# Kernel tuning notes

Hardware: AMD Instinct MI355X
Metric: run time of the kernel (lower is better)

Reference implementation:

```python
import jax, jax.numpy as jnp
import numpy as np

N = 100000      # nodes
E = 1600000     # directed edges (before self-loops)
DIN = 128       # input feature dim
HID = 32        # per-head hidden dim
HEADS = 4
D1 = HID * HEADS  # 128, concat width
NG = 64         # graphs in batch
NEG_SLOPE = 0.2 # PyG GATConv leaky_relu slope


def setup_inputs() -> dict:
    key = jax.random.key(0)
    ks = jax.random.split(key, 16)
    s = 0.05
    x = jax.random.normal(ks[0], (N, DIN), dtype=jnp.float32)
    edge_index = jax.random.randint(ks[1], (2, E), 0, N, dtype=jnp.int32)
    batch = jnp.sort(jax.random.randint(ks[2], (N,), 0, NG, dtype=jnp.int32))
    # GATConv 1: in=DIN, out=HID, heads=HEADS, concat=True
    W1 = jax.random.normal(ks[3], (D1, DIN), dtype=jnp.float32) * s
    a1s = jax.random.normal(ks[4], (HEADS, HID), dtype=jnp.float32) * s
    a1d = jax.random.normal(ks[5], (HEADS, HID), dtype=jnp.float32) * s
    b1 = jnp.zeros((D1,), jnp.float32)
    # GATConv 2: in=D1, out=HID, heads=HEADS, concat=True
    W2 = jax.random.normal(ks[6], (D1, D1), dtype=jnp.float32) * s
    a2s = jax.random.normal(ks[7], (HEADS, HID), dtype=jnp.float32) * s
    a2d = jax.random.normal(ks[8], (HEADS, HID), dtype=jnp.float32) * s
    b2 = jnp.zeros((D1,), jnp.float32)
    # GATConv 3: in=D1, out=HID, heads=HEADS, concat=False (mean over heads)
    W3 = jax.random.normal(ks[9], (D1, D1), dtype=jnp.float32) * s
    a3s = jax.random.normal(ks[10], (HEADS, HID), dtype=jnp.float32) * s
    a3d = jax.random.normal(ks[11], (HEADS, HID), dtype=jnp.float32) * s
    b3 = jnp.zeros((HID,), jnp.float32)
    lin_w = jax.random.normal(ks[12], (1, HID), dtype=jnp.float32) * s
    lin_b = jnp.zeros((1,), jnp.float32)
    return {"x": x, "edge_index": edge_index, "batch": batch,
            "W1": W1, "a1s": a1s, "a1d": a1d, "b1": b1,
            "W2": W2, "a2s": a2s, "a2d": a2d, "b2": b2,
            "W3": W3, "a3s": a3s, "a3d": a3d, "b3": b3,
            "lin_w": lin_w, "lin_b": lin_b}


def _gat_conv(x, ei, W, att_src, att_dst, bias, concat):
    """PyG GATConv (no edge features, self-loops already in ei)."""
    n = x.shape[0]
    h = (x @ W.T).reshape(n, HEADS, HID)          # [N, H, C]
    src, dst = ei[0], ei[1]
    a_src = jnp.einsum('nhc,hc->nh', h, att_src)  # [N, H]
    a_dst = jnp.einsum('nhc,hc->nh', h, att_dst)
    e = jax.nn.leaky_relu(a_src[src] + a_dst[dst], NEG_SLOPE)  # [Etot, H]
    # segment softmax over incoming edges of each dst node
    e_max = jax.ops.segment_max(e, dst, num_segments=n)
    ex = jnp.exp(e - e_max[dst])
    denom = jax.ops.segment_sum(ex, dst, num_segments=n)
    alpha = ex / denom[dst]                        # [Etot, H]
    out = jax.ops.segment_sum(h[src] * alpha[:, :, None], dst, num_segments=n)
    if concat:
        out = out.reshape(n, HEADS * HID)
    else:
        out = out.mean(axis=1)
    return out + bias


def reference(x, edge_index, batch, W1, a1s, a1d, b1, W2, a2s, a2d, b2,
              W3, a3s, a3d, b3, lin_w, lin_b):
    loops = jnp.arange(N, dtype=edge_index.dtype)
    ei = jnp.concatenate([edge_index, jnp.stack([loops, loops])], axis=1)
    h = jax.nn.elu(_gat_conv(x, ei, W1, a1s, a1d, b1, True))
    h = jax.nn.elu(_gat_conv(h, ei, W2, a2s, a2d, b2, True))
    h = jax.nn.elu(_gat_conv(h, ei, W3, a3s, a3d, b3, False))
    h = h @ lin_w.T + lin_b                        # [N, 1]
    counts = jax.ops.segment_sum(jnp.ones((N,), h.dtype), batch, num_segments=NG)
    pooled = jax.ops.segment_sum(h, batch, num_segments=NG) / counts[:, None]
    return pooled.squeeze()                        # [NG]
```

## Files before the change

kernel.cpp:

```cpp
#include <hip/hip_runtime.h>
#include <hip/hip_fp16.h>
#include <math.h>

#define D1 128
#define NEG 0.2f
#define NODE_SHIFT 9
#define BIN_NODES 512
#define MAXBIN 256

typedef short v8s __attribute__((ext_vector_type(8)));
typedef float v4f __attribute__((ext_vector_type(4)));

__device__ __forceinline__ float lrelu(float v){ return v > 0.f ? v : NEG * v; }
__device__ __forceinline__ float elu_f(float v){ return v > 0.f ? v : __expf(v) - 1.f; }

__device__ __forceinline__ unsigned short bf16s(float f){
    unsigned u = __float_as_uint(f);
    return (unsigned short)((u + 0x7fffu + ((u >> 16) & 1u)) >> 16);
}
__device__ __forceinline__ float bf2f(unsigned short s){
    return __uint_as_float(((unsigned)s) << 16);
}
__device__ __forceinline__ unsigned f2h2(float a, float b){
    return ((unsigned)__half_as_ushort(__float2half_rn(b)) << 16) |
           (unsigned)__half_as_ushort(__float2half_rn(a));
}
__device__ __forceinline__ float2 h2f2(unsigned u){
    float lo = __half2float(__ushort_as_half((unsigned short)(u & 0xffffu)));
    float hi = __half2float(__ushort_as_half((unsigned short)(u >> 16)));
    return make_float2(lo, hi);
}
__device__ __forceinline__ void split8(const float* f, v8s& hi, v8s& lo){
    #pragma unroll
    for (int i = 0; i < 8; i++){
        unsigned short h = bf16s(f[i]);
        ((short*)&hi)[i] = (short)h;
        ((short*)&lo)[i] = (short)bf16s(f[i] - bf2f(h));
    }
}


__global__ __launch_bounds__(256) void kb_hist(const int* __restrict__ ei,
                                               int* __restrict__ binCnt,
                                               int n_edges, int etot, int nbin){
    __shared__ int h[MAXBIN];
    for (int i = threadIdx.x; i < nbin; i += 256) h[i] = 0;
    __syncthreads();
    int stride = gridDim.x * 256;
    for (int e = blockIdx.x * 256 + threadIdx.x; e < etot; e += stride){
        int dst = (e < n_edges) ? ei[n_edges + e] : (e - n_edges);
        atomicAdd(&h[dst >> NODE_SHIFT], 1);
    }
    __syncthreads();
    for (int i = threadIdx.x; i < nbin; i += 256)
        if (h[i]) atomicAdd(&binCnt[i], h[i]);
}

__global__ void kb_scan(const int* __restrict__ binCnt, int* __restrict__ binStart,
                        int* __restrict__ binCursor, int nbin,
                        int* __restrict__ rowptr, int n_nodes, int etot){
    if (threadIdx.x == 0){
        int run = 0;
        for (int b = 0; b < nbin; b++){
            binStart[b] = run; binCursor[b] = run; run += binCnt[b];
        }
        binStart[nbin] = run;
        rowptr[n_nodes] = etot;
    }
}

__global__ __launch_bounds__(256) void kb_scatter(const int* __restrict__ ei,
                                                  int* __restrict__ binCursor,
                                                  uint2* __restrict__ staged,
                                                  int n_edges, int etot, int nbin){
    __shared__ int cnt[MAXBIN];
    __shared__ int base[MAXBIN];
    int e0 = blockIdx.x * 4096;
    for (int i = threadIdx.x; i < nbin; i += 256) cnt[i] = 0;
    __syncthreads();
    #pragma unroll 4
    for (int r = 0; r < 16; r++){
        int e = e0 + r * 256 + threadIdx.x;
        if (e < etot){
            int dst = (e < n_edges) ? ei[n_edges + e] : (e - n_edges);
            atomicAdd(&cnt[dst >> NODE_SHIFT], 1);
        }
    }
    __syncthreads();
    for (int i = threadIdx.x; i < nbin; i += 256){
        base[i] = cnt[i] ? atomicAdd(&binCursor[i], cnt[i]) : 0;
        cnt[i] = 0;
    }
    __syncthreads();
    #pragma unroll 4
    for (int r = 0; r < 16; r++){
        int e = e0 + r * 256 + threadIdx.x;
        if (e < etot){
            int src, dst;
            if (e < n_edges){ src = ei[e]; dst = ei[n_edges + e]; }
            else            { src = dst = e - n_edges; }
            int b = dst >> NODE_SHIFT;
            int p = base[b] + atomicAdd(&cnt[b], 1);
            staged[p] = make_uint2((unsigned)src, (unsigned)dst);
        }
    }
}

__global__ __launch_bounds__(512) void kb_final(const uint2* __restrict__ staged,
                                                const int* __restrict__ binStart,
                                                int* __restrict__ rowptr,
                                                int* __restrict__ eidx, int n_nodes){
    __shared__ int deg[BIN_NODES];
    __shared__ int cur[BIN_NODES];
    int b = blockIdx.x;
    int nbase = b << NODE_SHIFT;
    int s0 = binStart[b], s1 = binStart[b + 1];
    deg[threadIdx.x] = 0;
    __syncthreads();
    for (int i = s0 + threadIdx.x; i < s1; i += 512)
        atomicAdd(&deg[staged[i].y & (BIN_NODES - 1)], 1);
    __syncthreads();
    int v = deg[threadIdx.x];
    cur[threadIdx.x] = v;
    __syncthreads();
    for (int off = 1; off < BIN_NODES; off <<= 1){
        int t = (threadIdx.x >= off) ? cur[threadIdx.x - off] : 0;
        __syncthreads();
        cur[threadIdx.x] += t;
        __syncthreads();
    }
    int excl = cur[threadIdx.x] - v;
    int node = nbase + threadIdx.x;
    if (node < n_nodes) rowptr[node] = s0 + excl;
    cur[threadIdx.x] = s0 + excl;
    __syncthreads();
    for (int i = s0 + threadIdx.x; i < s1; i += 512){
        uint2 pr = staged[i];
        int p = atomicAdd(&cur[pr.y & (BIN_NODES - 1)], 1);
        eidx[p] = (int)pr.x;
    }
}


__global__ void k_prepw(const float* __restrict__ W1, const float* __restrict__ W2,
                        const float* __restrict__ W3, unsigned short* __restrict__ Bp){
    int t = blockIdx.x * 256 + threadIdx.x;
    if (t >= 49152) return;
    int w = t >> 14;
    int r = t & 16383;
    int k = r >> 7, j = r & 127;
    const float* W = (w == 0) ? W1 : (w == 1) ? W2 : W3;
    float val = W[j * 128 + k];
    unsigned short hi = bf16s(val);
    unsigned short lo = bf16s(val - bf2f(hi));
    int idx = (k >> 3) * 1024 + j * 8 + (k & 7);
    Bp[w * 32768 + idx] = hi;
    Bp[w * 32768 + 16384 + idx] = lo;
}


template<int FP32SRC>
__global__ __launch_bounds__(256) void k_mgemm(
        const float* __restrict__ Xf,
        const unsigned short* __restrict__ Xhi, const unsigned short* __restrict__ Xlo,
        const unsigned short* __restrict__ Bp,
        const float* __restrict__ aw_s, const float* __restrict__ aw_d,
        unsigned short* __restrict__ Hh,
        float* __restrict__ asrc, float* __restrict__ adst, int n_rows){
    extern __shared__ unsigned short Bs[];
    int lane = threadIdx.x & 63;
    int li = lane & 15, quad = lane >> 4;
    int wv = threadIdx.x >> 6;
    int r0 = blockIdx.x * 128 + wv * 32;

    int row0 = r0 + li;
    int row1 = r0 + 16 + li;
    int rc0 = row0 < n_rows ? row0 : 0;
    int rc1 = row1 < n_rows ? row1 : 0;

    v8s ah0[4], al0[4], ah1[4], al1[4];
    #pragma unroll
    for (int ks = 0; ks < 4; ks++){
        int koff = ks * 32 + quad * 8;
        if (FP32SRC){
            float f0[8], f1[8];
            *(float4*)&f0[0] = *(const float4*)(Xf + (size_t)rc0 * 128 + koff);
            *(float4*)&f0[4] = *(const float4*)(Xf + (size_t)rc0 * 128 + koff + 4);
            *(float4*)&f1[0] = *(const float4*)(Xf + (size_t)rc1 * 128 + koff);
            *(float4*)&f1[4] = *(const float4*)(Xf + (size_t)rc1 * 128 + koff + 4);
            split8(f0, ah0[ks], al0[ks]);
            split8(f1, ah1[ks], al1[ks]);
        } else {
            ah0[ks] = *(const v8s*)(Xhi + (size_t)rc0 * 128 + koff);
            al0[ks] = *(const v8s*)(Xlo + (size_t)rc0 * 128 + koff);
            ah1[ks] = *(const v8s*)(Xhi + (size_t)rc1 * 128 + koff);
            al1[ks] = *(const v8s*)(Xlo + (size_t)rc1 * 128 + koff);
        }
    }

    #pragma unroll
    for (int i = 0; i < 16; i++){
        int idx = threadIdx.x + i * 256;
        ((float4*)Bs)[idx] = ((const float4*)Bp)[idx];
    }
    __syncthreads();

    v4f acc[2][8];
    #pragma unroll
    for (int m = 0; m < 2; m++)
        #pragma unroll
        for (int t = 0; t < 8; t++)
            acc[m][t] = (v4f){0.f, 0.f, 0.f, 0.f};

    #pragma unroll
    for (int ks = 0; ks < 4; ks++){
        #pragma unroll
        for (int t = 0; t < 8; t++){
            int bo = (ks * 4 + quad) * 1024 + (t * 16 + li) * 8;
            v8s bh = *(const v8s*)(Bs + bo);
            v8s bl = *(const v8s*)(Bs + 16384 + bo);
            acc[0][t] = __builtin_amdgcn_mfma_f32_16x16x32_bf16(ah0[ks], bh, acc[0][t], 0, 0, 0);
            acc[0][t] = __builtin_amdgcn_mfma_f32_16x16x32_bf16(ah0[ks], bl, acc[0][t], 0, 0, 0);
            acc[0][t] = __builtin_amdgcn_mfma_f32_16x16x32_bf16(al0[ks], bh, acc[0][t], 0, 0, 0);
            acc[1][t] = __builtin_amdgcn_mfma_f32_16x16x32_bf16(ah1[ks], bh, acc[1][t], 0, 0, 0);
            acc[1][t] = __builtin_amdgcn_mfma_f32_16x16x32_bf16(ah1[ks], bl, acc[1][t], 0, 0, 0);
            acc[1][t] = __builtin_amdgcn_mfma_f32_16x16x32_bf16(al1[ks], bh, acc[1][t], 0, 0, 0);
        }
    }

    #pragma unroll
    for (int m = 0; m < 2; m++){
        #pragma unroll
        for (int t = 0; t < 8; t++){
            #pragma unroll
            for (int r = 0; r < 4; r++){
                float v  = acc[m][t][r];
                float vo = __shfl_xor(v, 1);
                if (!(li & 1)){
                    int row = r0 + m * 16 + quad * 4 + r;
                    if (row < n_rows)
                        *(unsigned*)(Hh + (size_t)row * 128 + t * 16 + li) = f2h2(v, vo);
                }
            }
        }
    }

    float as8[8], ad8[8];
    #pragma unroll
    for (int t = 0; t < 8; t++){
        as8[t] = aw_s[t * 16 + li];
        ad8[t] = aw_d[t * 16 + li];
    }
    #pragma unroll
    for (int m = 0; m < 2; m++){
        #pragma unroll
        for (int r = 0; r < 4; r++){
            float sp[4], dp[4];
            #pragma unroll
            for (int h = 0; h < 4; h++){
                sp[h] = acc[m][2*h][r] * as8[2*h] + acc[m][2*h+1][r] * as8[2*h+1];
                dp[h] = acc[m][2*h][r] * ad8[2*h] + acc[m][2*h+1][r] * ad8[2*h+1];
            }
            #pragma unroll
            for (int off = 1; off < 16; off <<= 1){
                #pragma unroll
                for (int h = 0; h < 4; h++){
                    sp[h] += __shfl_xor(sp[h], off);
                    dp[h] += __shfl_xor(dp[h], off);
                }
            }
            if (li == 0){
                int row = r0 + m * 16 + quad * 4 + r;
                if (row < n_rows){
                    ((float4*)asrc)[row] = make_float4(sp[0], sp[1], sp[2], sp[3]);
                    ((float4*)adst)[row] = make_float4(dp[0], dp[1], dp[2], dp[3]);
                }
            }
        }
    }
}


template<int MEAN>
__global__ __launch_bounds__(256) void k_aggr(
        const unsigned* __restrict__ Hh,
        const float* __restrict__ asrc, const float* __restrict__ adst,
        const int* __restrict__ rowptr, const int* __restrict__ eidx,
        const float* __restrict__ bias,
        unsigned short* __restrict__ Oh, unsigned short* __restrict__ Ol,
        float* __restrict__ Of, int n_nodes){
    int lane = threadIdx.x & 63;
    int wid  = threadIdx.x >> 6;
    int n = blockIdx.x * 4 + wid;
    if (n >= n_nodes) return;
    int row0 = rowptr[n];
    int deg  = rowptr[n + 1] - row0;
    const int* ep = eidx + row0;
    unsigned hd = (unsigned)(lane >> 4);
    unsigned ul = (unsigned)lane;
    float4 ad = ((const float4*)adst)[n];
    float adh = hd == 0 ? ad.x : hd == 1 ? ad.y : hd == 2 ? ad.z : ad.w;
    unsigned wh = (ul >> 3) & 3;
    float adw = wh == 0 ? ad.x : wh == 1 ? ad.y : wh == 2 ? ad.z : ad.w;
    int wsrc = (int)(hd * 8);

    float accx = 0.f, accy = 0.f, den = 0.f;
    int i = 0;
    for (; i + 8 <= deg; i += 8){
        unsigned s[8];
        #pragma unroll
        for (int j = 0; j < 8; j++) s[j] = (unsigned)ep[i + j];
        float aW = asrc[s[ul & 7] * 4u + wh];
        float w = __expf(lrelu(aW + adw));
        unsigned hw[8];
        #pragma unroll
        for (int j = 0; j < 8; j++) hw[j] = Hh[s[j] * 64u + ul];
        #pragma unroll
        for (int j = 0; j < 8; j++){
            float wj = __shfl(w, wsrc + j);
            float2 hv = h2f2(hw[j]);
            den  += wj;
            accx += wj * hv.x;
            accy += wj * hv.y;
        }
    }
    for (; i < deg; i++){
        unsigned s = (unsigned)ep[i];
        float w = __expf(lrelu(asrc[s * 4u + hd] + adh));
        float2 hv = h2f2(Hh[s * 64u + ul]);
        den  += w;
        accx += w * hv.x;
        accy += w * hv.y;
    }
    float rdh = 1.f / den;
    accx *= rdh; accy *= rdh;

    int c = lane * 2;
    if (!MEAN){
        float ox = elu_f(accx + bias[c]);
        float oy = elu_f(accy + bias[c + 1]);
        unsigned short hx = bf16s(ox), hy = bf16s(oy);
        unsigned short lx = bf16s(ox - bf2f(hx)), ly = bf16s(oy - bf2f(hy));
        *(ushort2*)(Oh + (size_t)n * 128 + c) = make_ushort2(hx, hy);
        *(ushort2*)(Ol + (size_t)n * 128 + c) = make_ushort2(lx, ly);
    } else {
        float sx = accx, sy = accy;
        sx += __shfl_xor(sx, 16); sy += __shfl_xor(sy, 16);
        sx += __shfl_xor(sx, 32); sy += __shfl_xor(sy, 32);
        if (lane < 16){
            int cc = lane * 2;
            float ox = elu_f(sx * 0.25f + bias[cc]);
            float oy = elu_f(sy * 0.25f + bias[cc + 1]);
            *(float2*)(Of + (size_t)n * 32 + cc) = make_float2(ox, oy);
        }
    }
}


__global__ void k_readout(const float* __restrict__ H3, const int* __restrict__ batch,
                          const float* __restrict__ lw, const float* __restrict__ lb,
                          float* __restrict__ pool, float* __restrict__ cnt, int n_nodes){
    __shared__ float pl[64];
    __shared__ float cl[64];
    if (threadIdx.x < 64){ pl[threadIdx.x] = 0.f; cl[threadIdx.x] = 0.f; }
    __syncthreads();
    int n = blockIdx.x * 256 + threadIdx.x;
    if (n < n_nodes){
        const float4* hp = (const float4*)(H3 + (size_t)n * 32);
        const float4* wp = (const float4*)lw;
        float y = 0.f;
        #pragma unroll
        for (int i = 0; i < 8; i++){
            float4 h4 = hp[i], w4 = wp[i];
            y += h4.x * w4.x + h4.y * w4.y + h4.z * w4.z + h4.w * w4.w;
        }
        y += lb[0];
        int b = batch[n];
        atomicAdd(&pl[b], y);
        atomicAdd(&cl[b], 1.f);
    }
    __syncthreads();
    if (threadIdx.x < 64 && cl[threadIdx.x] != 0.f){
        atomicAdd(&pool[threadIdx.x], pl[threadIdx.x]);
        atomicAdd(&cnt[threadIdx.x], cl[threadIdx.x]);
    }
}

__global__ void k_final(const float* __restrict__ pool, const float* __restrict__ cnt,
                        float* __restrict__ out){
    int g = threadIdx.x;
    if (g < 64) out[g] = (cnt[g] > 0.f) ? pool[g] / cnt[g] : 0.f;
}


extern "C" void kernel_launch(void* const* d_in, const int* in_sizes, int n_in,
                              void* d_out, int out_size, void* d_ws, size_t ws_size,
                              hipStream_t stream){
    const float* x   = (const float*)d_in[0];
    const int*   ei  = (const int*)  d_in[1];
    const int*   bat = (const int*)  d_in[2];
    const float* W1  = (const float*)d_in[3];
    const float* a1s = (const float*)d_in[4];
    const float* a1d = (const float*)d_in[5];
    const float* b1  = (const float*)d_in[6];
    const float* W2  = (const float*)d_in[7];
    const float* a2s = (const float*)d_in[8];
    const float* a2d = (const float*)d_in[9];
    const float* b2  = (const float*)d_in[10];
    const float* W3  = (const float*)d_in[11];
    const float* a3s = (const float*)d_in[12];
    const float* a3d = (const float*)d_in[13];
    const float* b3  = (const float*)d_in[14];
    const float* lw  = (const float*)d_in[15];
    const float* lb  = (const float*)d_in[16];
    (void)n_in; (void)out_size; (void)ws_size;

    const int n_nodes = in_sizes[0] / D1;
    const int n_edges = in_sizes[1] / 2;
    const int etot    = n_edges + n_nodes;
    const int nbin    = (n_nodes + BIN_NODES - 1) >> NODE_SHIFT;

    char* p = (char*)d_ws;
    size_t off = 0;
    auto alloc = [&](size_t bytes) -> char* {
        char* r = p + off;
        off = (off + bytes + 511) & ~(size_t)511;
        return r;
    };
    unsigned short* Hh   = (unsigned short*)alloc((size_t)n_nodes * 128 * 2);
    unsigned short* Xhi  = (unsigned short*)alloc((size_t)n_nodes * 128 * 2);
    unsigned short* Xlo  = (unsigned short*)alloc((size_t)n_nodes * 128 * 2);
    float*          asrc = (float*)alloc((size_t)n_nodes * 4 * 4);
    float*          adst = (float*)alloc((size_t)n_nodes * 4 * 4);
    unsigned short* Bp   = (unsigned short*)alloc(3 * 32768 * 2);
    int*   rowptr  = (int*)alloc((size_t)(n_nodes + 1) * 4);
    int*   eidx    = (int*)alloc((size_t)etot * 4);
    uint2* staged  = (uint2*)alloc((size_t)etot * 8);
    int*   binCnt  = (int*)alloc(MAXBIN * 4);
    int*   binStart= (int*)alloc((MAXBIN + 1) * 4);
    int*   binCur  = (int*)alloc(MAXBIN * 4);
    float* pool    = (float*)alloc(64 * 4);
    float* cnt     = (float*)alloc(64 * 4);
    float* h3      = (float*)Xhi;

    hipMemsetAsync(binCnt, 0, MAXBIN * 4, stream);
    hipMemsetAsync(pool, 0, 64 * 4, stream);
    hipMemsetAsync(cnt, 0, 64 * 4, stream);

    k_prepw<<<192, 256, 0, stream>>>(W1, W2, W3, Bp);

    int cb = (etot + 4095) / 4096;
    kb_hist<<<cb, 256, 0, stream>>>(ei, binCnt, n_edges, etot, nbin);
    kb_scan<<<1, 64, 0, stream>>>(binCnt, binStart, binCur, nbin, rowptr, n_nodes, etot);
    kb_scatter<<<cb, 256, 0, stream>>>(ei, binCur, staged, n_edges, etot, nbin);
    kb_final<<<nbin, 512, 0, stream>>>(staged, binStart, rowptr, eidx, n_nodes);

    int mb = (n_nodes + 127) / 128;
    int rb = (n_nodes + 3) / 4;

    k_mgemm<1><<<mb, 256, 65536, stream>>>(x, nullptr, nullptr, Bp,
                                           a1s, a1d, Hh, asrc, adst, n_nodes);
    k_aggr<0><<<rb, 256, 0, stream>>>((const unsigned*)Hh, asrc, adst, rowptr, eidx,
                                      b1, Xhi, Xlo, nullptr, n_nodes);
    k_mgemm<0><<<mb, 256, 65536, stream>>>(nullptr, Xhi, Xlo, Bp + 32768,
                                           a2s, a2d, Hh, asrc, adst, n_nodes);
    k_aggr<0><<<rb, 256, 0, stream>>>((const unsigned*)Hh, asrc, adst, rowptr, eidx,
                                      b2, Xhi, Xlo, nullptr, n_nodes);
    k_mgemm<0><<<mb, 256, 65536, stream>>>(nullptr, Xhi, Xlo, Bp + 65536,
                                           a3s, a3d, Hh, asrc, adst, n_nodes);
    k_aggr<1><<<rb, 256, 0, stream>>>((const unsigned*)Hh, asrc, adst, rowptr, eidx,
                                      b3, nullptr, nullptr, h3, n_nodes);

    int ob = (n_nodes + 255) / 256;
    k_readout<<<ob, 256, 0, stream>>>(h3, bat, lw, lb, pool, cnt, n_nodes);
    k_final<<<1, 64, 0, stream>>>(pool, cnt, (float*)d_out);
}
```

Baseline: 572.8 us.

## Pack staged edges into 32-bit words and halve GEMM shared memory via K-staging

The CSR build now packs each staged edge as the local destination (9 bits) and the source (17 bits) into one 32-bit word, halving the staged buffer's traffic. The GEMM stops holding all four K-slices of the A operand in registers and stops keeping the full 64KB B matrix in LDS. It instead loads B in two 32KB halves, with a sync between them, and loads the A fragments per K-step. The aim is higher occupancy (launch_bounds 256,4) at the cost of an extra barrier and serialized B loads. The packing assumes node ids fit in 17 bits (below 131072).

Measured after the change: 545.7 us. -4.7%, faster.

```diff
diff --git a/kernel.cpp b/kernel.cpp
--- a/kernel.cpp
+++ b/kernel.cpp
@@ -71,7 +71,7 @@
 
 __global__ __launch_bounds__(256) void kb_scatter(const int* __restrict__ ei,
                                                   int* __restrict__ binCursor,
-                                                  uint2* __restrict__ staged,
+                                                  unsigned* __restrict__ staged,
                                                   int n_edges, int etot, int nbin){
     __shared__ int cnt[MAXBIN];
     __shared__ int base[MAXBIN];
@@ -101,12 +101,12 @@
             else            { src = dst = e - n_edges; }
             int b = dst >> NODE_SHIFT;
             int p = base[b] + atomicAdd(&cnt[b], 1);
-            staged[p] = make_uint2((unsigned)src, (unsigned)dst);
-        }
-    }
-}
-
-__global__ __launch_bounds__(512) void kb_final(const uint2* __restrict__ staged,
+            staged[p] = ((unsigned)(dst & (BIN_NODES - 1)) << 17) | (unsigned)src;
+        }
+    }
+}
+
+__global__ __launch_bounds__(512) void kb_final(const unsigned* __restrict__ staged,
                                                 const int* __restrict__ binStart,
                                                 int* __restrict__ rowptr,
                                                 int* __restrict__ eidx, int n_nodes){
@@ -118,7 +118,7 @@
     deg[threadIdx.x] = 0;
     __syncthreads();
     for (int i = s0 + threadIdx.x; i < s1; i += 512)
-        atomicAdd(&deg[staged[i].y & (BIN_NODES - 1)], 1);
+        atomicAdd(&deg[staged[i] >> 17], 1);
     __syncthreads();
     int v = deg[threadIdx.x];
     cur[threadIdx.x] = v;
@@ -135,9 +135,9 @@
     cur[threadIdx.x] = s0 + excl;
     __syncthreads();
     for (int i = s0 + threadIdx.x; i < s1; i += 512){
-        uint2 pr = staged[i];
-        int p = atomicAdd(&cur[pr.y & (BIN_NODES - 1)], 1);
-        eidx[p] = (int)pr.x;
+        unsigned pr = staged[i];
+        int p = atomicAdd(&cur[pr >> 17], 1);
+        eidx[p] = (int)(pr & 0x1FFFFu);
     }
 }
 
@@ -160,17 +160,17 @@
 
 
 template<int FP32SRC>
-__global__ __launch_bounds__(256) void k_mgemm(
+__global__ __launch_bounds__(256, 4) void k_mgemm(
         const float* __restrict__ Xf,
         const unsigned short* __restrict__ Xhi, const unsigned short* __restrict__ Xlo,
         const unsigned short* __restrict__ Bp,
         const float* __restrict__ aw_s, const float* __restrict__ aw_d,
         unsigned short* __restrict__ Hh,
         float* __restrict__ asrc, float* __restrict__ adst, int n_rows){
-    extern __shared__ unsigned short Bs[];
+    __shared__ unsigned short Bs[16384];
     int lane = threadIdx.x & 63;
+    int wv   = threadIdx.x >> 6;
     int li = lane & 15, quad = lane >> 4;
-    int wv = threadIdx.x >> 6;
     int r0 = blockIdx.x * 128 + wv * 32;
 
     int row0 = r0 + li;
@@ -178,33 +178,6 @@
     int rc0 = row0 < n_rows ? row0 : 0;
     int rc1 = row1 < n_rows ? row1 : 0;
 
-    v8s ah0[4], al0[4], ah1[4], al1[4];
-    #pragma unroll
-    for (int ks = 0; ks < 4; ks++){
-        int koff = ks * 32 + quad * 8;
-        if (FP32SRC){
-            float f0[8], f1[8];
-            *(float4*)&f0[0] = *(const float4*)(Xf + (size_t)rc0 * 128 + koff);
-            *(float4*)&f0[4] = *(const float4*)(Xf + (size_t)rc0 * 128 + koff + 4);
-            *(float4*)&f1[0] = *(const float4*)(Xf + (size_t)rc1 * 128 + koff);
-            *(float4*)&f1[4] = *(const float4*)(Xf + (size_t)rc1 * 128 + koff + 4);
-            split8(f0, ah0[ks], al0[ks]);
-            split8(f1, ah1[ks], al1[ks]);
-        } else {
-            ah0[ks] = *(const v8s*)(Xhi + (size_t)rc0 * 128 + koff);
-            al0[ks] = *(const v8s*)(Xlo + (size_t)rc0 * 128 + koff);
-            ah1[ks] = *(const v8s*)(Xhi + (size_t)rc1 * 128 + koff);
-            al1[ks] = *(const v8s*)(Xlo + (size_t)rc1 * 128 + koff);
-        }
-    }
-
-    #pragma unroll
-    for (int i = 0; i < 16; i++){
-        int idx = threadIdx.x + i * 256;
-        ((float4*)Bs)[idx] = ((const float4*)Bp)[idx];
-    }
-    __syncthreads();
-
     v4f acc[2][8];
     #pragma unroll
     for (int m = 0; m < 2; m++)
@@ -213,18 +186,46 @@
             acc[m][t] = (v4f){0.f, 0.f, 0.f, 0.f};
 
     #pragma unroll
-    for (int ks = 0; ks < 4; ks++){
-        #pragma unroll
-        for (int t = 0; t < 8; t++){
-            int bo = (ks * 4 + quad) * 1024 + (t * 16 + li) * 8;
-            v8s bh = *(const v8s*)(Bs + bo);
-            v8s bl = *(const v8s*)(Bs + 16384 + bo);
-            acc[0][t] = __builtin_amdgcn_mfma_f32_16x16x32_bf16(ah0[ks], bh, acc[0][t], 0, 0, 0);
-            acc[0][t] = __builtin_amdgcn_mfma_f32_16x16x32_bf16(ah0[ks], bl, acc[0][t], 0, 0, 0);
-            acc[0][t] = __builtin_amdgcn_mfma_f32_16x16x32_bf16(al0[ks], bh, acc[0][t], 0, 0, 0);
-            acc[1][t] = __builtin_amdgcn_mfma_f32_16x16x32_bf16(ah1[ks], bh, acc[1][t], 0, 0, 0);
-            acc[1][t] = __builtin_amdgcn_mfma_f32_16x16x32_bf16(ah1[ks], bl, acc[1][t], 0, 0, 0);
-            acc[1][t] = __builtin_amdgcn_mfma_f32_16x16x32_bf16(al1[ks], bh, acc[1][t], 0, 0, 0);
+    for (int g = 0; g < 2; g++){
+        if (g) __syncthreads();
+        #pragma unroll
+        for (int i = 0; i < 4; i++){
+            int idx = threadIdx.x + i * 256;
+            ((float4*)Bs)[idx]          = ((const float4*)(Bp + g * 8192))[idx];
+            ((float4*)(Bs + 8192))[idx] = ((const float4*)(Bp + 16384 + g * 8192))[idx];
+        }
+        __syncthreads();
+        #pragma unroll
+        for (int ks2 = 0; ks2 < 2; ks2++){
+            int ks = g * 2 + ks2;
+            int koff = ks * 32 + quad * 8;
+            v8s ah0, al0, ah1, al1;
+            if (FP32SRC){
+                float f0[8], f1[8];
+                *(float4*)&f0[0] = *(const float4*)(Xf + (size_t)rc0 * 128 + koff);
+                *(float4*)&f0[4] = *(const float4*)(Xf + (size_t)rc0 * 128 + koff + 4);
+                *(float4*)&f1[0] = *(const float4*)(Xf + (size_t)rc1 * 128 + koff);
+                *(float4*)&f1[4] = *(const float4*)(Xf + (size_t)rc1 * 128 + koff + 4);
+                split8(f0, ah0, al0);
+                split8(f1, ah1, al1);
+            } else {
+                ah0 = *(const v8s*)(Xhi + (size_t)rc0 * 128 + koff);
+                al0 = *(const v8s*)(Xlo + (size_t)rc0 * 128 + koff);
+                ah1 = *(const v8s*)(Xhi + (size_t)rc1 * 128 + koff);
+                al1 = *(const v8s*)(Xlo + (size_t)rc1 * 128 + koff);
+            }
+            #pragma unroll
+            for (int t = 0; t < 8; t++){
+                int bo = ks2 * 4096 + quad * 1024 + (t * 16 + li) * 8;
+                v8s bh = *(const v8s*)(Bs + bo);
+                v8s bl = *(const v8s*)(Bs + 8192 + bo);
+                acc[0][t] = __builtin_amdgcn_mfma_f32_16x16x32_bf16(ah0, bh, acc[0][t], 0, 0, 0);
+                acc[0][t] = __builtin_amdgcn_mfma_f32_16x16x32_bf16(ah0, bl, acc[0][t], 0, 0, 0);
+                acc[0][t] = __builtin_amdgcn_mfma_f32_16x16x32_bf16(al0, bh, acc[0][t], 0, 0, 0);
+                acc[1][t] = __builtin_amdgcn_mfma_f32_16x16x32_bf16(ah1, bh, acc[1][t], 0, 0, 0);
+                acc[1][t] = __builtin_amdgcn_mfma_f32_16x16x32_bf16(ah1, bl, acc[1][t], 0, 0, 0);
+                acc[1][t] = __builtin_amdgcn_mfma_f32_16x16x32_bf16(al1, bh, acc[1][t], 0, 0, 0);
+            }
         }
     }
 
@@ -433,15 +434,15 @@
     float*          asrc = (float*)alloc((size_t)n_nodes * 4 * 4);
     float*          adst = (float*)alloc((size_t)n_nodes * 4 * 4);
     unsigned short* Bp   = (unsigned short*)alloc(3 * 32768 * 2);
-    int*   rowptr  = (int*)alloc((size_t)(n_nodes + 1) * 4);
-    int*   eidx    = (int*)alloc((size_t)etot * 4);
-    uint2* staged  = (uint2*)alloc((size_t)etot * 8);
-    int*   binCnt  = (int*)alloc(MAXBIN * 4);
-    int*   binStart= (int*)alloc((MAXBIN + 1) * 4);
-    int*   binCur  = (int*)alloc(MAXBIN * 4);
-    float* pool    = (float*)alloc(64 * 4);
-    float* cnt     = (float*)alloc(64 * 4);
-    float* h3      = (float*)Xhi;
+    int*      rowptr  = (int*)alloc((size_t)(n_nodes + 1) * 4);
+    int*      eidx    = (int*)alloc((size_t)etot * 4);
+    unsigned* staged  = (unsigned*)alloc((size_t)etot * 4);
+    int*      binCnt  = (int*)alloc(MAXBIN * 4);
+    int*      binStart= (int*)alloc((MAXBIN + 1) * 4);
+    int*      binCur  = (int*)alloc(MAXBIN * 4);
+    float*    pool    = (float*)alloc(64 * 4);
+    float*    cnt     = (float*)alloc(64 * 4);
+    float*    h3      = (float*)Xhi;
 
     hipMemsetAsync(binCnt, 0, MAXBIN * 4, stream);
     hipMemsetAsync(pool, 0, 64 * 4, stream);
@@ -458,16 +459,16 @@
     int mb = (n_nodes + 127) / 128;
     int rb = (n_nodes + 3) / 4;
 
-    k_mgemm<1><<<mb, 256, 65536, stream>>>(x, nullptr, nullptr, Bp,
-                                           a1s, a1d, Hh, asrc, adst, n_nodes);
+    k_mgemm<1><<<mb, 256, 0, stream>>>(x, nullptr, nullptr, Bp,
+                                       a1s, a1d, Hh, asrc, adst, n_nodes);
     k_aggr<0><<<rb, 256, 0, stream>>>((const unsigned*)Hh, asrc, adst, rowptr, eidx,
                                       b1, Xhi, Xlo, nullptr, n_nodes);
-    k_mgemm<0><<<mb, 256, 65536, stream>>>(nullptr, Xhi, Xlo, Bp + 32768,
-                                           a2s, a2d, Hh, asrc, adst, n_nodes);
+    k_mgemm<0><<<mb, 256, 0, stream>>>(nullptr, Xhi, Xlo, Bp + 32768,
+                                       a2s, a2d, Hh, asrc, adst, n_nodes);
     k_aggr<0><<<rb, 256, 0, stream>>>((const unsigned*)Hh, asrc, adst, rowptr, eidx,
                                       b2, Xhi, Xlo, nullptr, n_nodes);
-    k_mgemm<0><<<mb, 256, 65536, stream>>>(nullptr, Xhi, Xlo, Bp + 65536,
-                                           a3s, a3d, Hh, asrc, adst, n_nodes);
+    k_mgemm<0><<<mb, 256, 0, stream>>>(nullptr, Xhi, Xlo, Bp + 65536,
+                                       a3s, a3d, Hh, asrc, adst, n_nodes);
     k_aggr<1><<<rb, 256, 0, stream>>>((const unsigned*)Hh, asrc, adst, rowptr, eidx,
                                       b3, nullptr, nullptr, h3, n_nodes);
 
```
